# Kernel optimization log

Measured on AMD Instinct MI355X. Metric: run time of the kernel, lower is better.

Reference implementation:

```python
import jax, jax.numpy as jnp
import numpy as np

N = 50000      # nodes
E2 = 400000    # undirected edges
E = 2 * E2     # directed edges (each undirected edge in both directions)
DIN = 512      # input feature dim
DH = 128       # MLP hidden
C = 8          # num classes / BP channels


def setup_inputs() -> dict:
    key = jax.random.key(0)
    ks = jax.random.split(key, 9)
    x = jax.random.normal(ks[0], (N, DIN), jnp.float32)
    src0 = jax.random.randint(ks[1], (E2,), 0, N)
    dst0 = jax.random.randint(ks[2], (E2,), 0, N)
    # symmetric directed edge list: row 0 = source j, row 1 = target i
    edge_index = jnp.stack([jnp.concatenate([src0, dst0]),
                            jnp.concatenate([dst0, src0])])
    w0 = jax.random.uniform(ks[3], (E2,), jnp.float32, 0.5, 1.5)
    edge_weight = jnp.concatenate([w0, w0])  # reverse edge shares weight
    # edge_rv[e] = index of the reverse of edge e
    edge_rv = jnp.concatenate([jnp.arange(E2) + E2, jnp.arange(E2)])
    W1 = jax.random.normal(ks[4], (DIN, DH), jnp.float32) * 0.05
    b1 = jnp.zeros((DH,), jnp.float32)
    W2 = jax.random.normal(ks[5], (DH, C), jnp.float32) * 0.05
    b2 = jnp.zeros((C,), jnp.float32)
    param = jax.random.normal(ks[6], (C, C), jnp.float32) * 0.1
    return {"x": x, "edge_index": edge_index, "edge_weight": edge_weight,
            "edge_rv": edge_rv, "W1": W1, "b1": b1, "W2": W2, "b2": b2,
            "param": param, "K": 5}


def log_normalize(log_x):
    return log_x - jax.nn.logsumexp(log_x, axis=-1, keepdims=True)


def reference(x, edge_index, edge_weight, edge_rv, W1, b1, W2, b2, param, K):
    # MLP transform + LogSoftmax -> initial log-beliefs [N, C]
    h = jax.nn.relu(x @ W1 + b1)
    log_b0 = jax.nn.log_softmax(h @ W2 + b2, axis=-1)

    # learn_H=True: logH = logsigmoid(param + param^T), [C, C]
    logH = jax.nn.log_sigmoid(param + param.T)
    src, dst = edge_index[0], edge_index[1]
    # per-edge coupling matrix [E, C, C]
    logC = edge_weight[:, None, None] * logH[None, :, :]

    log_b = log_b0
    log_msg = None
    for _ in range(K):
        x_j = log_b[src]                       # gather source beliefs [E, C]
        if log_msg is not None:
            x_j = x_j - log_msg[edge_rv]       # remove reverse message
        # tropical-semiring matvec in log domain: logsumexp over source channel
        log_msg = log_normalize(jax.nn.logsumexp(x_j[:, :, None] + logC, axis=1))
        agg = jax.ops.segment_sum(log_msg, dst, num_segments=N)  # scatter-add
        log_b = log_normalize(log_b0 + agg)
    return log_b
```

## Files before the change

### kernel.cpp

```cpp
#include <hip/hip_runtime.h>
#include <hip/hip_bf16.h>
#include <hip/hip_fp16.h>
#include <math.h>

#define NN 50000
#define EE 800000
#define E2K 400000
#define DINK 512
#define DHK 128
#define CK 8
#define KIT 5
#define NBLKS 196
#define NPB 32

typedef __attribute__((ext_vector_type(8))) short short8;
typedef __attribute__((ext_vector_type(4))) float f32x4;

__device__ __forceinline__ unsigned short f2bf(float f) {
    union { float f; unsigned int u; } v;
    v.f = f;
    unsigned int u = v.u;
    unsigned int r = (u + 0x7FFFu + ((u >> 16) & 1u)) >> 16;
    return (unsigned short)r;
}
__device__ __forceinline__ float bfu2f(unsigned int lo16) {
    union { unsigned int u; float f; } v;
    v.u = lo16 << 16;
    return v.f;
}

__global__ __launch_bounds__(256) void prep_kernel(
    const float* __restrict__ W1, const float* __restrict__ param,
    unsigned short* __restrict__ W1t, float* __restrict__ logH) {
    if (blockIdx.x < 256) {
        int idx = blockIdx.x * 256 + threadIdx.x;
        int n = idx >> 9;
        int k = idx & 511;
        W1t[idx] = f2bf(W1[(size_t)k * DHK + n]);
    } else if (threadIdx.x < 64) {
        int t = threadIdx.x;
        int i = t >> 3, j = t & 7;
        float z = param[i * 8 + j] + param[j * 8 + i];
        logH[t] = fminf(z, 0.0f) - log1pf(expf(-fabsf(z)));
    }
}

__global__ __launch_bounds__(256) void mlp_mfma_kernel(
    const float* __restrict__ x, const unsigned short* __restrict__ W1t,
    const float* __restrict__ b1, const float* __restrict__ W2,
    const float* __restrict__ b2, float* __restrict__ logb0) {
    __shared__ unsigned short hs[128 * 136];
    __shared__ float W2s[128 * 8];
    __shared__ float b1s[128];
    __shared__ float b2s[8];

    const int tid = threadIdx.x;
    const int wave = tid >> 6;
    const int lane = tid & 63;
    const int q = lane >> 4;
    const int lm = lane & 15;
    const int wm = wave >> 1, wn = wave & 1;
    const int n0 = blockIdx.x * 128;

    if (tid < 128) b1s[tid] = b1[tid];
    if (tid < 8) b2s[tid] = b2[tid];
    {
        int i = tid * 4;
        *(float4*)&W2s[i] = *(const float4*)&W2[i];
    }
    __syncthreads();

    const float* xptr[4];
#pragma unroll
    for (int mt = 0; mt < 4; ++mt) {
        int r = n0 + wm * 64 + mt * 16 + lm;
        if (r > NN - 1) r = NN - 1;
        xptr[mt] = x + (size_t)r * DINK + q * 8;
    }
    const unsigned short* bptr[4];
#pragma unroll
    for (int nt = 0; nt < 4; ++nt) {
        int c = wn * 64 + nt * 16 + lm;
        bptr[nt] = W1t + (size_t)c * DINK + q * 8;
    }

    f32x4 acc[4][4];
#pragma unroll
    for (int mt = 0; mt < 4; ++mt)
#pragma unroll
        for (int nt = 0; nt < 4; ++nt) acc[mt][nt] = (f32x4){0.f, 0.f, 0.f, 0.f};

    float4 ar[4][2];
    short8 bc[4];
#pragma unroll
    for (int mt = 0; mt < 4; ++mt) {
        ar[mt][0] = *(const float4*)(xptr[mt]);
        ar[mt][1] = *(const float4*)(xptr[mt] + 4);
    }
#pragma unroll
    for (int nt = 0; nt < 4; ++nt) bc[nt] = *(const short8*)(bptr[nt]);

#pragma unroll
    for (int k0 = 32; k0 <= DINK; k0 += 32) {
        float4 ar2[4][2];
        short8 b2f[4];
        if (k0 < DINK) {
#pragma unroll
            for (int mt = 0; mt < 4; ++mt) {
                ar2[mt][0] = *(const float4*)(xptr[mt] + k0);
                ar2[mt][1] = *(const float4*)(xptr[mt] + k0 + 4);
            }
#pragma unroll
            for (int nt = 0; nt < 4; ++nt)
                b2f[nt] = *(const short8*)(bptr[nt] + k0);
        }
        short8 af[4];
#pragma unroll
        for (int mt = 0; mt < 4; ++mt) {
            union { short8 s; __hip_bfloat162 h[4]; } cv;
            cv.h[0] = __float22bfloat162_rn(make_float2(ar[mt][0].x, ar[mt][0].y));
            cv.h[1] = __float22bfloat162_rn(make_float2(ar[mt][0].z, ar[mt][0].w));
            cv.h[2] = __float22bfloat162_rn(make_float2(ar[mt][1].x, ar[mt][1].y));
            cv.h[3] = __float22bfloat162_rn(make_float2(ar[mt][1].z, ar[mt][1].w));
            af[mt] = cv.s;
        }
#pragma unroll
        for (int mt = 0; mt < 4; ++mt)
#pragma unroll
            for (int nt = 0; nt < 4; ++nt)
                acc[mt][nt] = __builtin_amdgcn_mfma_f32_16x16x32_bf16(
                    af[mt], bc[nt], acc[mt][nt], 0, 0, 0);
        if (k0 < DINK) {
#pragma unroll
            for (int mt = 0; mt < 4; ++mt) {
                ar[mt][0] = ar2[mt][0];
                ar[mt][1] = ar2[mt][1];
            }
#pragma unroll
            for (int nt = 0; nt < 4; ++nt) bc[nt] = b2f[nt];
        }
    }

#pragma unroll
    for (int nt = 0; nt < 4; ++nt) {
        int j = wn * 64 + nt * 16 + lm;
        float bj = b1s[j];
#pragma unroll
        for (int mt = 0; mt < 4; ++mt) {
            int rbase = wm * 64 + mt * 16 + q * 4;
#pragma unroll
            for (int r = 0; r < 4; ++r) {
                float h = fmaxf(acc[mt][nt][r] + bj, 0.0f);
                hs[(rbase + r) * 136 + j] = f2bf(h);
            }
        }
    }
    __syncthreads();

    int row = tid >> 1;
    int half = tid & 1;
    const unsigned short* hp = &hs[row * 136 + half * 64];
    float p[8] = {0.f, 0.f, 0.f, 0.f, 0.f, 0.f, 0.f, 0.f};
#pragma unroll
    for (int ch = 0; ch < 8; ++ch) {
        uint4 c4 = *(const uint4*)(hp + ch * 8);
        unsigned int uu[4] = {c4.x, c4.y, c4.z, c4.w};
#pragma unroll
        for (int p2 = 0; p2 < 4; ++p2) {
            float h0 = bfu2f(uu[p2] & 0xFFFFu);
            float h1 = bfu2f(uu[p2] >> 16);
            int j = half * 64 + ch * 8 + p2 * 2;
            const float* w0 = &W2s[j * 8];
            const float* w1 = &W2s[(j + 1) * 8];
#pragma unroll
            for (int c = 0; c < 8; ++c) p[c] = fmaf(h0, w0[c], p[c]);
#pragma unroll
            for (int c = 0; c < 8; ++c) p[c] = fmaf(h1, w1[c], p[c]);
        }
    }
#pragma unroll
    for (int c = 0; c < 8; ++c) p[c] += __shfl_xor(p[c], 1, 64);
    int grow = n0 + row;
    if (half == 0 && grow < NN) {
        float v[8];
        float mx = -1e30f;
#pragma unroll
        for (int c = 0; c < 8; ++c) {
            v[c] = p[c] + b2s[c];
            mx = fmaxf(mx, v[c]);
        }
        float s = 0.0f;
#pragma unroll
        for (int c = 0; c < 8; ++c) s += expf(v[c] - mx);
        float ln = mx + logf(s);
        float4* p0 = (float4*)&logb0[(size_t)grow * 8];
        p0[0] = make_float4(v[0] - ln, v[1] - ln, v[2] - ln, v[3] - ln);
        p0[1] = make_float4(v[4] - ln, v[5] - ln, v[6] - ln, v[7] - ln);
    }
}


__global__ __launch_bounds__(256) void deg_pair_kernel(const int* __restrict__ ei,
                                                       int* __restrict__ cnt) {
    int e = blockIdx.x * 256 + threadIdx.x;
    if (e >= E2K) return;
    int s = ei[e];
    int d = ei[EE + e];
    atomicAdd(&cnt[d], 1);
    atomicAdd(&cnt[s], 1);
}

__global__ __launch_bounds__(256) void scan_partial_kernel(
    const int* __restrict__ cnt, int* __restrict__ partial) {
    __shared__ int sd[256];
    int t = threadIdx.x;
    int i = blockIdx.x * 256 + t;
    sd[t] = (i < NN) ? cnt[i] : 0;
    __syncthreads();
#pragma unroll
    for (int s = 128; s > 0; s >>= 1) {
        if (t < s) sd[t] += sd[t + s];
        __syncthreads();
    }
    if (t == 0) partial[blockIdx.x] = sd[0];
}

__global__ __launch_bounds__(256) void scan_tops_kernel(
    const int* __restrict__ partial, int* __restrict__ tops) {
    __shared__ int sd[256];
    int t = threadIdx.x;
    sd[t] = (t < NBLKS) ? partial[t] : 0;
    __syncthreads();
#pragma unroll
    for (int s = 1; s < 256; s <<= 1) {
        int a = sd[t];
        int b = (t >= s) ? sd[t - s] : 0;
        __syncthreads();
        sd[t] = a + b;
        __syncthreads();
    }
    if (t < NBLKS) tops[t] = (t > 0) ? sd[t - 1] : 0;
}

__global__ __launch_bounds__(256) void scan_write_kernel(
    const int* __restrict__ cnt, const int* __restrict__ tops,
    int* __restrict__ off) {
    __shared__ int sd[256];
    int t = threadIdx.x;
    int i = blockIdx.x * 256 + t;
    int v = (i < NN) ? cnt[i] : 0;
    sd[t] = v;
    __syncthreads();
#pragma unroll
    for (int s = 1; s < 256; s <<= 1) {
        int a = sd[t];
        int b = (t >= s) ? sd[t - s] : 0;
        __syncthreads();
        sd[t] = a + b;
        __syncthreads();
    }
    if (i < NN) off[i] = tops[blockIdx.x] + sd[t] - v;
    if (i == NN - 1) off[NN] = EE;
}

__global__ __launch_bounds__(256) void pos_pair_kernel(
    const int* __restrict__ ei, const float* __restrict__ ew,
    const int* __restrict__ off, int* __restrict__ cnt,
    int* __restrict__ perm_src, float* __restrict__ perm_w,
    int* __restrict__ perm_dst, int* __restrict__ perm_rvp) {
    int e = blockIdx.x * 256 + threadIdx.x;
    if (e >= E2K) return;
    int s = ei[e];
    int d = ei[EE + e];
    float w = ew[e];
    int pA = off[d] + atomicAdd(&cnt[d], 1);
    int pB = off[s] + atomicAdd(&cnt[s], 1);
    perm_src[pA] = s;
    perm_src[pB] = d;
    perm_w[pA] = w;
    perm_w[pB] = w;
    perm_dst[pA] = d;
    perm_dst[pB] = s;
    perm_rvp[pA] = pB;
    perm_rvp[pB] = pA;
}


__global__ __launch_bounds__(256) void edge_msg_kernel(
    const int* __restrict__ perm_src, const float* __restrict__ perm_w,
    const float* __restrict__ logH, const float* __restrict__ logb0,
    const uint4* __restrict__ xin16, uint4* __restrict__ msg16, int first) {
    __shared__ float lH[64];
    if (threadIdx.x < 64) lH[threadIdx.x] = logH[threadIdx.x];
    __syncthreads();
    int p = blockIdx.x * 256 + threadIdx.x;
    if (p >= EE) return;

    float w = perm_w[p];
    float xj[8];
    if (first) {
        int s = perm_src[p];
        const float4* pb = (const float4*)&logb0[(size_t)s * 8];
        float4 v0 = pb[0], v1 = pb[1];
        xj[0] = v0.x; xj[1] = v0.y; xj[2] = v0.z; xj[3] = v0.w;
        xj[4] = v1.x; xj[5] = v1.y; xj[6] = v1.z; xj[7] = v1.w;
    } else {
        union { uint4 u; _Float16 h[8]; } cv;
        cv.u = xin16[p];
#pragma unroll
        for (int c = 0; c < 8; ++c) xj[c] = (float)cv.h[c];
    }

    float M = xj[0];
#pragma unroll
    for (int c = 1; c < 8; ++c) M = fmaxf(M, xj[c]);
#pragma unroll
    for (int c = 0; c < 8; ++c) xj[c] -= M;

    float mg[8];
#pragma unroll
    for (int c2 = 0; c2 < 8; ++c2) {
        float ssum = 0.0f;
#pragma unroll
        for (int c1 = 0; c1 < 8; ++c1)
            ssum += __expf(fmaf(w, lH[c1 * 8 + c2], xj[c1]));
        mg[c2] = __logf(ssum);
    }
    float mm = mg[0];
#pragma unroll
    for (int c = 1; c < 8; ++c) mm = fmaxf(mm, mg[c]);
    float se = 0.0f;
#pragma unroll
    for (int c = 0; c < 8; ++c) se += __expf(mg[c] - mm);
    float ln = mm + __logf(se);

    union { uint4 u; _Float16 h[8]; } ov;
#pragma unroll
    for (int c = 0; c < 8; ++c) ov.h[c] = (_Float16)(mg[c] - ln);
    msg16[p] = ov.u;
}

__global__ __launch_bounds__(256) void node_fused_kernel(
    const float* __restrict__ logb0, const int* __restrict__ off,
    const uint4* __restrict__ msg16, const int* __restrict__ perm_dst,
    const int* __restrict__ perm_rvp, uint4* __restrict__ xin16,
    float* __restrict__ out, int last) {
    __shared__ float sb[NPB * 8];
    const int n0 = blockIdx.x * NPB;
    const int t = threadIdx.x;
    const int nl = t >> 3;
    const int c = t & 7;
    const int n = n0 + nl;
    const _Float16* msgh = (const _Float16*)msg16;

    if (n < NN) {
        int j0 = off[n], j1 = off[n + 1];
        float a = logb0[(size_t)n * 8 + c];
        for (int j = j0; j < j1; ++j) a += (float)msgh[(size_t)j * 8 + c];
        float mx = a;
#pragma unroll
        for (int s = 1; s < 8; s <<= 1) mx = fmaxf(mx, __shfl_xor(mx, s, 8));
        float sum = __expf(a - mx);
#pragma unroll
        for (int s = 1; s < 8; s <<= 1) sum += __shfl_xor(sum, s, 8);
        float v = a - (mx + __logf(sum));
        if (last) out[(size_t)n * 8 + c] = v;
        sb[nl * 8 + c] = v;
    }
    if (last) return;
    __syncthreads();

    _Float16* xinh = (_Float16*)xin16;
    const int nend = (n0 + NPB < NN) ? (n0 + NPB) : NN;
    const int jb0 = off[n0];
    const int jb1 = off[nend];
    const int items = (jb1 - jb0) * 8;
    for (int item = t; item < items; item += 256) {
        int j = jb0 + (item >> 3);
        int c2 = item & 7;
        int dl = perm_dst[j] - n0;
        float val = sb[dl * 8 + c2] - (float)msgh[(size_t)j * 8 + c2];
        xinh[(size_t)perm_rvp[j] * 8 + c2] = (_Float16)val;
    }
}

extern "C" void kernel_launch(void* const* d_in, const int* in_sizes, int n_in,
                              void* d_out, int out_size, void* d_ws, size_t ws_size,
                              hipStream_t stream) {
    const float* x = (const float*)d_in[0];
    const int* ei = (const int*)d_in[1];
    const float* ew = (const float*)d_in[2];
    const float* W1 = (const float*)d_in[4];
    const float* b1 = (const float*)d_in[5];
    const float* W2 = (const float*)d_in[6];
    const float* b2 = (const float*)d_in[7];
    const float* param = (const float*)d_in[8];
    float* out = (float*)d_out;

    float* wsf = (float*)d_ws;
    float* logH = wsf;
    float* logb0 = logH + 64;
    uint4* msg16 = (uint4*)(logb0 + (size_t)NN * 8);
    uint4* xin16 = msg16 + EE;
    int* off = (int*)(xin16 + EE);
    int* perm_src = off + (NN + 1);
    float* perm_w = (float*)(perm_src + EE);
    int* perm_rvp = (int*)(perm_w + EE);
    int* perm_dst = perm_rvp + EE;
    unsigned short* W1t = (unsigned short*)(perm_dst + EE);
    int* cnt = (int*)xin16;
    int* partial = cnt + NN;
    int* tops = partial + NBLKS;

    prep_kernel<<<257, 256, 0, stream>>>(W1, param, W1t, logH);
    mlp_mfma_kernel<<<(NN + 127) / 128, 256, 0, stream>>>(x, W1t, b1, W2, b2,
                                                          logb0);

    const int EB = (EE + 255) / 256;
    const int E2B = (E2K + 255) / 256;

    hipMemsetAsync(cnt, 0, (size_t)NN * sizeof(int), stream);
    deg_pair_kernel<<<E2B, 256, 0, stream>>>(ei, cnt);
    scan_partial_kernel<<<NBLKS, 256, 0, stream>>>(cnt, partial);
    scan_tops_kernel<<<1, 256, 0, stream>>>(partial, tops);
    scan_write_kernel<<<NBLKS, 256, 0, stream>>>(cnt, tops, off);
    hipMemsetAsync(cnt, 0, (size_t)NN * sizeof(int), stream);
    pos_pair_kernel<<<E2B, 256, 0, stream>>>(ei, ew, off, cnt, perm_src,
                                             perm_w, perm_dst, perm_rvp);

    const int NB = (NN + NPB - 1) / NPB;
    for (int it = 0; it < KIT; ++it) {
        int first = (it == 0) ? 1 : 0;
        int last = (it == KIT - 1) ? 1 : 0;
        edge_msg_kernel<<<EB, 256, 0, stream>>>(perm_src, perm_w, logH, logb0,
                                                xin16, msg16, first);
        node_fused_kernel<<<NB, 256, 0, stream>>>(logb0, off, msg16, perm_dst,
                                                  perm_rvp, xin16, out, last);
    }
}
```

Measured before the change: 479.5 us.

## Fuse edge message and node update into one per-iteration BP kernel

Merges the per-edge message kernel and the per-node aggregation/reverse-message kernel into a single kernel per iteration. Messages for a 32-node block's incoming edges are computed and staged in shared memory (up to 1024 edges), so the msg16 global round-trip disappears. xin is now double-buffered to avoid read/write races across blocks. Edge metadata is packed into two int2 arrays to cut separate index loads. Blocks whose edge range exceeds the cap recompute messages in a second pass, and per-block work becomes uneven with fewer threads per edge.

New measurement: 432.2 us. -9.9%, faster.

```diff
diff --git a/kernel.cpp b/kernel.cpp
--- a/kernel.cpp
+++ b/kernel.cpp
@@ -12,6 +12,7 @@
 #define KIT 5
 #define NBLKS 196
 #define NPB 32
+#define CAP 1024
 
 typedef __attribute__((ext_vector_type(8))) short short8;
 typedef __attribute__((ext_vector_type(4))) float f32x4;
@@ -266,121 +267,173 @@
 __global__ __launch_bounds__(256) void pos_pair_kernel(
     const int* __restrict__ ei, const float* __restrict__ ew,
     const int* __restrict__ off, int* __restrict__ cnt,
-    int* __restrict__ perm_src, float* __restrict__ perm_w,
-    int* __restrict__ perm_dst, int* __restrict__ perm_rvp) {
+    int2* __restrict__ perm_sw, int2* __restrict__ perm_dr) {
     int e = blockIdx.x * 256 + threadIdx.x;
     if (e >= E2K) return;
     int s = ei[e];
     int d = ei[EE + e];
-    float w = ew[e];
+    int wbits = __float_as_int(ew[e]);
     int pA = off[d] + atomicAdd(&cnt[d], 1);
     int pB = off[s] + atomicAdd(&cnt[s], 1);
-    perm_src[pA] = s;
-    perm_src[pB] = d;
-    perm_w[pA] = w;
-    perm_w[pB] = w;
-    perm_dst[pA] = d;
-    perm_dst[pB] = s;
-    perm_rvp[pA] = pB;
-    perm_rvp[pB] = pA;
-}
-
-
-__global__ __launch_bounds__(256) void edge_msg_kernel(
-    const int* __restrict__ perm_src, const float* __restrict__ perm_w,
-    const float* __restrict__ logH, const float* __restrict__ logb0,
-    const uint4* __restrict__ xin16, uint4* __restrict__ msg16, int first) {
+    int2 v;
+    v.x = s; v.y = wbits; perm_sw[pA] = v;
+    v.x = d;              perm_sw[pB] = v;
+    v.x = d; v.y = pB;    perm_dr[pA] = v;
+    v.x = s; v.y = pA;    perm_dr[pB] = v;
+}
+
+__global__ __launch_bounds__(256) void bp_iter_kernel(
+    const float* __restrict__ logb0, const int* __restrict__ off,
+    const int2* __restrict__ perm_sw, const int2* __restrict__ perm_dr,
+    const float* __restrict__ logH, const uint4* __restrict__ xin_cur,
+    uint4* __restrict__ xin_next, float* __restrict__ out,
+    int first, int last) {
+    __shared__ _Float16 smg[CAP * 8];
+    __shared__ float sb[NPB * 8];
     __shared__ float lH[64];
-    if (threadIdx.x < 64) lH[threadIdx.x] = logH[threadIdx.x];
-    __syncthreads();
-    int p = blockIdx.x * 256 + threadIdx.x;
-    if (p >= EE) return;
-
-    float w = perm_w[p];
-    float xj[8];
-    if (first) {
-        int s = perm_src[p];
-        const float4* pb = (const float4*)&logb0[(size_t)s * 8];
-        float4 v0 = pb[0], v1 = pb[1];
-        xj[0] = v0.x; xj[1] = v0.y; xj[2] = v0.z; xj[3] = v0.w;
-        xj[4] = v1.x; xj[5] = v1.y; xj[6] = v1.z; xj[7] = v1.w;
-    } else {
-        union { uint4 u; _Float16 h[8]; } cv;
-        cv.u = xin16[p];
-#pragma unroll
-        for (int c = 0; c < 8; ++c) xj[c] = (float)cv.h[c];
-    }
-
-    float M = xj[0];
-#pragma unroll
-    for (int c = 1; c < 8; ++c) M = fmaxf(M, xj[c]);
-#pragma unroll
-    for (int c = 0; c < 8; ++c) xj[c] -= M;
-
-    float mg[8];
-#pragma unroll
-    for (int c2 = 0; c2 < 8; ++c2) {
-        float ssum = 0.0f;
-#pragma unroll
-        for (int c1 = 0; c1 < 8; ++c1)
-            ssum += __expf(fmaf(w, lH[c1 * 8 + c2], xj[c1]));
-        mg[c2] = __logf(ssum);
-    }
-    float mm = mg[0];
-#pragma unroll
-    for (int c = 1; c < 8; ++c) mm = fmaxf(mm, mg[c]);
-    float se = 0.0f;
-#pragma unroll
-    for (int c = 0; c < 8; ++c) se += __expf(mg[c] - mm);
-    float ln = mm + __logf(se);
-
-    union { uint4 u; _Float16 h[8]; } ov;
-#pragma unroll
-    for (int c = 0; c < 8; ++c) ov.h[c] = (_Float16)(mg[c] - ln);
-    msg16[p] = ov.u;
-}
-
-__global__ __launch_bounds__(256) void node_fused_kernel(
-    const float* __restrict__ logb0, const int* __restrict__ off,
-    const uint4* __restrict__ msg16, const int* __restrict__ perm_dst,
-    const int* __restrict__ perm_rvp, uint4* __restrict__ xin16,
-    float* __restrict__ out, int last) {
-    __shared__ float sb[NPB * 8];
+    const int t = threadIdx.x;
+    if (t < 64) lH[t] = logH[t];
+
     const int n0 = blockIdx.x * NPB;
-    const int t = threadIdx.x;
+    const int nend = (n0 + NPB < NN) ? (n0 + NPB) : NN;
+    const int jb0 = off[n0];
+    const int jb1 = off[nend];
     const int nl = t >> 3;
     const int c = t & 7;
     const int n = n0 + nl;
-    const _Float16* msgh = (const _Float16*)msg16;
-
-    if (n < NN) {
-        int j0 = off[n], j1 = off[n + 1];
-        float a = logb0[(size_t)n * 8 + c];
-        for (int j = j0; j < j1; ++j) a += (float)msgh[(size_t)j * 8 + c];
-        float mx = a;
-#pragma unroll
-        for (int s = 1; s < 8; s <<= 1) mx = fmaxf(mx, __shfl_xor(mx, s, 8));
-        float sum = __expf(a - mx);
-#pragma unroll
-        for (int s = 1; s < 8; s <<= 1) sum += __shfl_xor(sum, s, 8);
-        float v = a - (mx + __logf(sum));
+
+    float a = 0.0f;
+    int jn0 = 0, jn1 = 0;
+    if (n < nend) {
+        jn0 = off[n];
+        jn1 = off[n + 1];
+        a = logb0[(size_t)n * 8 + c];
+    }
+    __syncthreads();
+
+    const int single = (jb1 - jb0) <= CAP;
+
+    for (int cb = jb0; cb < jb1; cb += CAP) {
+        int ce = (cb + CAP < jb1) ? (cb + CAP) : jb1;
+        for (int j = cb + t; j < ce; j += 256) {
+            int2 sw = perm_sw[j];
+            float w = __int_as_float(sw.y);
+            float xj[8];
+            if (first) {
+                const float4* pb = (const float4*)&logb0[(size_t)sw.x * 8];
+                float4 v0 = pb[0], v1 = pb[1];
+                xj[0] = v0.x; xj[1] = v0.y; xj[2] = v0.z; xj[3] = v0.w;
+                xj[4] = v1.x; xj[5] = v1.y; xj[6] = v1.z; xj[7] = v1.w;
+            } else {
+                union { uint4 u; _Float16 h[8]; } cv;
+                cv.u = xin_cur[j];
+#pragma unroll
+                for (int k = 0; k < 8; ++k) xj[k] = (float)cv.h[k];
+            }
+            float M = xj[0];
+#pragma unroll
+            for (int k = 1; k < 8; ++k) M = fmaxf(M, xj[k]);
+#pragma unroll
+            for (int k = 0; k < 8; ++k) xj[k] -= M;
+            float mg[8];
+#pragma unroll
+            for (int c2 = 0; c2 < 8; ++c2) {
+                float ssum = 0.0f;
+#pragma unroll
+                for (int c1 = 0; c1 < 8; ++c1)
+                    ssum += __expf(fmaf(w, lH[c1 * 8 + c2], xj[c1]));
+                mg[c2] = __logf(ssum);
+            }
+            float mm = mg[0];
+#pragma unroll
+            for (int k = 1; k < 8; ++k) mm = fmaxf(mm, mg[k]);
+            float se = 0.0f;
+#pragma unroll
+            for (int k = 0; k < 8; ++k) se += __expf(mg[k] - mm);
+            float ln = mm + __logf(se);
+            union { uint4 u; _Float16 h[8]; } ov;
+#pragma unroll
+            for (int k = 0; k < 8; ++k) ov.h[k] = (_Float16)(mg[k] - ln);
+            *(uint4*)&smg[(j - cb) * 8] = ov.u;
+        }
+        __syncthreads();
+        int lo = (jn0 > cb) ? jn0 : cb;
+        int hi = (jn1 < ce) ? jn1 : ce;
+        for (int j = lo; j < hi; ++j) a += (float)smg[(j - cb) * 8 + c];
+        __syncthreads();
+    }
+
+    float mx = a;
+#pragma unroll
+    for (int s = 1; s < 8; s <<= 1) mx = fmaxf(mx, __shfl_xor(mx, s, 8));
+    float sum = __expf(a - mx);
+#pragma unroll
+    for (int s = 1; s < 8; s <<= 1) sum += __shfl_xor(sum, s, 8);
+    float v = a - (mx + __logf(sum));
+    if (n < nend) {
         if (last) out[(size_t)n * 8 + c] = v;
         sb[nl * 8 + c] = v;
     }
     if (last) return;
     __syncthreads();
 
-    _Float16* xinh = (_Float16*)xin16;
-    const int nend = (n0 + NPB < NN) ? (n0 + NPB) : NN;
-    const int jb0 = off[n0];
-    const int jb1 = off[nend];
-    const int items = (jb1 - jb0) * 8;
-    for (int item = t; item < items; item += 256) {
-        int j = jb0 + (item >> 3);
-        int c2 = item & 7;
-        int dl = perm_dst[j] - n0;
-        float val = sb[dl * 8 + c2] - (float)msgh[(size_t)j * 8 + c2];
-        xinh[(size_t)perm_rvp[j] * 8 + c2] = (_Float16)val;
+    for (int cb = jb0; cb < jb1; cb += CAP) {
+        int ce = (cb + CAP < jb1) ? (cb + CAP) : jb1;
+        if (!single) {
+            for (int j = cb + t; j < ce; j += 256) {
+                int2 sw = perm_sw[j];
+                float w = __int_as_float(sw.y);
+                float xj[8];
+                if (first) {
+                    const float4* pb = (const float4*)&logb0[(size_t)sw.x * 8];
+                    float4 v0 = pb[0], v1 = pb[1];
+                    xj[0] = v0.x; xj[1] = v0.y; xj[2] = v0.z; xj[3] = v0.w;
+                    xj[4] = v1.x; xj[5] = v1.y; xj[6] = v1.z; xj[7] = v1.w;
+                } else {
+                    union { uint4 u; _Float16 h[8]; } cv;
+                    cv.u = xin_cur[j];
+#pragma unroll
+                    for (int k = 0; k < 8; ++k) xj[k] = (float)cv.h[k];
+                }
+                float M = xj[0];
+#pragma unroll
+                for (int k = 1; k < 8; ++k) M = fmaxf(M, xj[k]);
+#pragma unroll
+                for (int k = 0; k < 8; ++k) xj[k] -= M;
+                float mg[8];
+#pragma unroll
+                for (int c2 = 0; c2 < 8; ++c2) {
+                    float ssum = 0.0f;
+#pragma unroll
+                    for (int c1 = 0; c1 < 8; ++c1)
+                        ssum += __expf(fmaf(w, lH[c1 * 8 + c2], xj[c1]));
+                    mg[c2] = __logf(ssum);
+                }
+                float mm = mg[0];
+#pragma unroll
+                for (int k = 1; k < 8; ++k) mm = fmaxf(mm, mg[k]);
+                float se = 0.0f;
+#pragma unroll
+                for (int k = 0; k < 8; ++k) se += __expf(mg[k] - mm);
+                float ln = mm + __logf(se);
+                union { uint4 u; _Float16 h[8]; } ov;
+#pragma unroll
+                for (int k = 0; k < 8; ++k) ov.h[k] = (_Float16)(mg[k] - ln);
+                *(uint4*)&smg[(j - cb) * 8] = ov.u;
+            }
+            __syncthreads();
+        }
+        _Float16* xinh = (_Float16*)xin_next;
+        int items = (ce - cb) * 8;
+        for (int item = t; item < items; item += 256) {
+            int j = cb + (item >> 3);
+            int c2 = item & 7;
+            int2 dr = perm_dr[j];
+            int dl = dr.x - n0;
+            float val = sb[dl * 8 + c2] - (float)smg[(j - cb) * 8 + c2];
+            xinh[(size_t)dr.y * 8 + c2] = (_Float16)val;
+        }
+        if (!single) __syncthreads();
     }
 }
 
@@ -400,15 +453,13 @@
     float* wsf = (float*)d_ws;
     float* logH = wsf;
     float* logb0 = logH + 64;
-    uint4* msg16 = (uint4*)(logb0 + (size_t)NN * 8);
-    uint4* xin16 = msg16 + EE;
-    int* off = (int*)(xin16 + EE);
-    int* perm_src = off + (NN + 1);
-    float* perm_w = (float*)(perm_src + EE);
-    int* perm_rvp = (int*)(perm_w + EE);
-    int* perm_dst = perm_rvp + EE;
-    unsigned short* W1t = (unsigned short*)(perm_dst + EE);
-    int* cnt = (int*)xin16;
+    uint4* xinA = (uint4*)(logb0 + (size_t)NN * 8);
+    uint4* xinB = xinA + EE;
+    int* off = (int*)(xinB + EE);
+    int2* perm_sw = (int2*)(off + (NN + 1));
+    int2* perm_dr = perm_sw + EE;
+    unsigned short* W1t = (unsigned short*)(perm_dr + EE);
+    int* cnt = (int*)xinA;
     int* partial = cnt + NN;
     int* tops = partial + NBLKS;
 
@@ -416,7 +467,6 @@
     mlp_mfma_kernel<<<(NN + 127) / 128, 256, 0, stream>>>(x, W1t, b1, W2, b2,
                                                           logb0);
 
-    const int EB = (EE + 255) / 256;
     const int E2B = (E2K + 255) / 256;
 
     hipMemsetAsync(cnt, 0, (size_t)NN * sizeof(int), stream);
@@ -425,16 +475,15 @@
     scan_tops_kernel<<<1, 256, 0, stream>>>(partial, tops);
     scan_write_kernel<<<NBLKS, 256, 0, stream>>>(cnt, tops, off);
     hipMemsetAsync(cnt, 0, (size_t)NN * sizeof(int), stream);
-    pos_pair_kernel<<<E2B, 256, 0, stream>>>(ei, ew, off, cnt, perm_src,
-                                             perm_w, perm_dst, perm_rvp);
+    pos_pair_kernel<<<E2B, 256, 0, stream>>>(ei, ew, off, cnt, perm_sw, perm_dr);
 
     const int NB = (NN + NPB - 1) / NPB;
+    uint4* cur = xinA;
+    uint4* nxt = xinB;
     for (int it = 0; it < KIT; ++it) {
-        int first = (it == 0) ? 1 : 0;
-        int last = (it == KIT - 1) ? 1 : 0;
-        edge_msg_kernel<<<EB, 256, 0, stream>>>(perm_src, perm_w, logH, logb0,
-                                                xin16, msg16, first);
-        node_fused_kernel<<<NB, 256, 0, stream>>>(logb0, off, msg16, perm_dst,
-                                                  perm_rvp, xin16, out, last);
-    }
-}
+        bp_iter_kernel<<<NB, 256, 0, stream>>>(
+            logb0, off, perm_sw, perm_dr, logH, cur, nxt, out,
+            it == 0 ? 1 : 0, it == KIT - 1 ? 1 : 0);
+        uint4* tmp = cur; cur = nxt; nxt = tmp;
+    }
+}
```
